# Performance work log

Measured on AMD Instinct MI355X. Metric: run time of the kernel, lower is better.

The kernel has to match this reference:

```python
import jax, jax.numpy as jnp
import numpy as np

B, T, V, D = 2048, 32, 1024, 256


def setup_inputs() -> dict:
    key = jax.random.key(0)
    k1, k2 = jax.random.split(key)
    input = jax.random.normal(k1, (B, T, D), dtype=jnp.float32)
    codebook = jax.random.normal(k2, (T, V, D), dtype=jnp.float32)
    return {"input": input, "codebook": codebook}


def reference(input, codebook):
    # input: [B, T, D]; codebook: [T, V, D]
    x = jnp.moveaxis(input, 1, 0)  # [T, B, D]
    # Squared euclidean distances; argmin is invariant to the sqrt in cdist.
    x2 = jnp.sum(x * x, axis=-1)[..., None]            # [T, B, 1]
    c2 = jnp.sum(codebook * codebook, axis=-1)[:, None, :]  # [T, 1, V]
    xc = jnp.einsum('tbd,tvd->tbv', x, codebook)       # [T, B, V]
    d2 = x2 - 2.0 * xc + c2                            # [T, B, V]
    idxes_ = jnp.argmin(d2, axis=-1)                   # [T, B]
    idxes = idxes_.T                                   # [B, T]
    # Direct per-token gather: embed[b, t] = codebook[t, idxes[b, t]]
    embed_ = codebook[jnp.arange(T)[:, None], idxes_]  # [T, B, D]
    embed = jnp.moveaxis(embed_, 0, 1)                 # [B, T, D]
    return embed, idxes
```

## Files before the change

kernel.cpp:

```cpp
#include <hip/hip_runtime.h>
#include <hip/hip_bf16.h>


#define B_ 2048
#define T_ 32
#define V_ 1024
#define D_ 256
#define BT 128
#define VT 128
#define NVT 8
#define CAND_MAX 1280
#define MARGIN 8.0f

typedef __attribute__((ext_vector_type(8))) short short8;
typedef __attribute__((ext_vector_type(4))) float f32x4;

__device__ __forceinline__ unsigned short f2bf(float f) {
    unsigned u = __builtin_bit_cast(unsigned, f);
    unsigned r = u + 0x7FFFu + ((u >> 16) & 1u);
    return (unsigned short)(r >> 16);
}

__device__ __forceinline__ short8 pack8(float4 a, float4 b) {
    short8 r;
    r[0] = (short)f2bf(a.x); r[1] = (short)f2bf(a.y);
    r[2] = (short)f2bf(a.z); r[3] = (short)f2bf(a.w);
    r[4] = (short)f2bf(b.x); r[5] = (short)f2bf(b.y);
    r[6] = (short)f2bf(b.z); r[7] = (short)f2bf(b.w);
    return r;
}

__global__ void prep_kernel(const float* __restrict__ cb, float* __restrict__ c2,
                            unsigned short* __restrict__ cbb) {
    const int wave = threadIdx.x >> 6, lane = threadIdx.x & 63;
    const int row = blockIdx.x * 4 + wave;
    const float4 v4 = *(const float4*)(cb + (size_t)row * D_ + lane * 4);
    float s = v4.x * v4.x + v4.y * v4.y + v4.z * v4.z + v4.w * v4.w;
    #pragma unroll
    for (int off = 32; off; off >>= 1) s += __shfl_down(s, off, 64);
    if (lane == 0) c2[row] = s;

    ushort4 b4;
    b4.x = f2bf(v4.x); b4.y = f2bf(v4.y); b4.z = f2bf(v4.z); b4.w = f2bf(v4.w);
    *(ushort4*)(cbb + (size_t)row * D_ + lane * 4) = b4;
}

__global__ void c2_kernel(const float* __restrict__ cb, float* __restrict__ c2) {
    const int row = blockIdx.x * 4 + (threadIdx.x >> 6);
    const int lane = threadIdx.x & 63;
    const float4 v = ((const float4*)(cb + (size_t)row * D_))[lane];
    float s = v.x * v.x + v.y * v.y + v.z * v.z + v.w * v.w;
    #pragma unroll
    for (int off = 32; off; off >>= 1) s += __shfl_down(s, off, 64);
    if (lane == 0) c2[row] = s;
}

__global__ __launch_bounds__(256, 2)
void vq_kernel(const float* __restrict__ x, const float* __restrict__ cb,
               const float* __restrict__ c2, const unsigned short* __restrict__ cbb,
               float* __restrict__ out, int use_bf) {
    const int t  = blockIdx.x;
    const int b0 = blockIdx.y * BT;

    __shared__ short8 A_lds[4096];
    __shared__ float  minPart[BT * 2];
    __shared__ unsigned long long result[BT];
    __shared__ unsigned s_cand[CAND_MAX];
    __shared__ unsigned s_cnt;

    const int tid = threadIdx.x;
    const int wave = tid >> 6, lane = tid & 63;
    const int wm = wave & 1, wn = wave >> 1;
    const int q = lane >> 4, ln = lane & 15;

    if (tid < BT) result[tid] = ~0ULL;
    minPart[tid] = 3.4e38f;
    if (tid == 0) s_cnt = 0;

    #pragma unroll
    for (int i = 0; i < 16; ++i) {
        int gid = i * 256 + tid, r = gid >> 5, g = gid & 31;
        const float4* src = (const float4*)(x + (((size_t)(b0 + r)) * T_ + t) * D_ + g * 8);
        A_lds[r * 32 + (g ^ (r & 15))] = pack8(src[0], src[1]);
    }

    const unsigned short* bb = cbb + ((size_t)t * V_ + wn * 64 + ln) * D_ + q * 8;
    const float*          fb = cb  + ((size_t)t * V_ + wn * 64 + ln) * D_ + q * 8;

    auto loadB = [&](int vt, int kc, short8 (&dst)[4]) {
        #pragma unroll
        for (int nt = 0; nt < 4; ++nt) {
            const int off = (vt * VT + nt * 16) * D_ + kc * 32;
            if (use_bf) {
                dst[nt] = *(const short8*)(bb + off);
            } else {
                const float4* s = (const float4*)(fb + off);
                dst[nt] = pack8(s[0], s[1]);
            }
        }
    };

    short8 bA[4], bB[4];
    loadB(0, 0, bA);
    __syncthreads();

    const int abase = (wm * 64 + ln) * 32;

    for (int vt = 0; vt < NVT; ++vt) {
        f32x4 acc[4][4];
        #pragma unroll
        for (int mt = 0; mt < 4; ++mt)
            #pragma unroll
            for (int nt = 0; nt < 4; ++nt) acc[mt][nt] = (f32x4){0.f, 0.f, 0.f, 0.f};

        #pragma unroll
        for (int kh = 0; kh < 4; ++kh) {
            const int kc0 = kh * 2, kc1 = kh * 2 + 1;

            loadB(vt, kc1, bB);
            {
                short8 af[4];
                #pragma unroll
                for (int mt = 0; mt < 4; ++mt)
                    af[mt] = A_lds[abase + mt * 512 + ((kc0 * 4 + q) ^ ln)];
                #pragma unroll
                for (int mt = 0; mt < 4; ++mt)
                    #pragma unroll
                    for (int nt = 0; nt < 4; ++nt)
                        acc[mt][nt] = __builtin_amdgcn_mfma_f32_16x16x32_bf16(af[mt], bA[nt], acc[mt][nt], 0, 0, 0);
            }
            if (!(vt == NVT - 1 && kh == 3)) {
                int nv = vt, nk = kc0 + 2;
                if (kh == 3) { nv = vt + 1; nk = 0; }
                loadB(nv, nk, bA);
            }
            {
                short8 af[4];
                #pragma unroll
                for (int mt = 0; mt < 4; ++mt)
                    af[mt] = A_lds[abase + mt * 512 + ((kc1 * 4 + q) ^ ln)];
                #pragma unroll
                for (int mt = 0; mt < 4; ++mt)
                    #pragma unroll
                    for (int nt = 0; nt < 4; ++nt)
                        acc[mt][nt] = __builtin_amdgcn_mfma_f32_16x16x32_bf16(af[mt], bB[nt], acc[mt][nt], 0, 0, 0);
            }
        }

        const float* c2p = c2 + t * V_ + vt * VT + wn * 64 + ln;
        float cc[4];
        #pragma unroll
        for (int nt = 0; nt < 4; ++nt) cc[nt] = c2p[nt * 16];

        #pragma unroll
        for (int mt = 0; mt < 4; ++mt)
            #pragma unroll
            for (int i = 0; i < 4; ++i) {
                float mn = 3.4e38f;
                #pragma unroll
                for (int nt = 0; nt < 4; ++nt)
                    mn = fminf(mn, fmaf(-2.0f, acc[mt][nt][i], cc[nt]));
                mn = fminf(mn, __shfl_xor(mn, 1, 64));
                mn = fminf(mn, __shfl_xor(mn, 2, 64));
                mn = fminf(mn, __shfl_xor(mn, 4, 64));
                mn = fminf(mn, __shfl_xor(mn, 8, 64));
                if (ln == 0) {
                    int r = wm * 64 + mt * 16 + q * 4 + i;
                    minPart[r * 2 + wn] = fminf(minPart[r * 2 + wn], mn);
                }
            }
        __syncthreads();

        #pragma unroll
        for (int mt = 0; mt < 4; ++mt)
            #pragma unroll
            for (int i = 0; i < 4; ++i) {
                int r = wm * 64 + mt * 16 + q * 4 + i;
                float2 mp = *(const float2*)&minPart[r * 2];
                float thr = fminf(mp.x, mp.y) + MARGIN;
                #pragma unroll
                for (int nt = 0; nt < 4; ++nt) {
                    float s = fmaf(-2.0f, acc[mt][nt][i], cc[nt]);
                    if (s < thr) {
                        int v = vt * VT + wn * 64 + nt * 16 + ln;
                        unsigned pos = atomicAdd(&s_cnt, 1u);
                        if (pos < CAND_MAX) s_cand[pos] = (unsigned)((r << 10) | v);
                    }
                }
            }
    }

    __syncthreads();
    const unsigned ncand = min(s_cnt, (unsigned)CAND_MAX);
    const int grp = tid >> 4, l16 = tid & 15;
    for (unsigned ci = grp; ci < ncand; ci += 16) {
        const unsigned e = s_cand[ci];
        const int row = e >> 10, v = e & 1023;
        const float* xr = x + (((size_t)(b0 + row)) * T_ + t) * D_ + l16 * 16;
        const float* cr = cb + ((size_t)t * V_ + v) * D_ + l16 * 16;
        float dot = 0.f;
        #pragma unroll
        for (int j = 0; j < 4; ++j) {
            float4 a = *(const float4*)(xr + j * 4);
            float4 b = *(const float4*)(cr + j * 4);
            dot = fmaf(a.x, b.x, dot); dot = fmaf(a.y, b.y, dot);
            dot = fmaf(a.z, b.z, dot); dot = fmaf(a.w, b.w, dot);
        }
        dot += __shfl_xor(dot, 1, 64);
        dot += __shfl_xor(dot, 2, 64);
        dot += __shfl_xor(dot, 4, 64);
        dot += __shfl_xor(dot, 8, 64);
        if (l16 == 0) {
            float sc = fmaf(-2.0f, dot, c2[t * V_ + v]);
            unsigned u = __builtin_bit_cast(unsigned, sc);
            u = (u & 0x80000000u) ? ~u : (u | 0x80000000u);
            atomicMin(&result[row], ((unsigned long long)u << 32) | (unsigned)v);
        }
    }
    __syncthreads();

    if (tid < BT)
        out[(size_t)B_ * T_ * D_ + (size_t)(b0 + tid) * T_ + t] =
            (float)(int)(result[tid] & 1023u);

    const int w = tid >> 6, gl = tid & 63;
    #pragma unroll
    for (int i = 0; i < 32; ++i) {
        const int row = w * 32 + i;
        const int idx = (int)(result[row] & 1023u);
        const float4 src = *(const float4*)(cb + ((size_t)t * V_ + idx) * D_ + gl * 4);
        *(float4*)(out + (((size_t)(b0 + row)) * T_ + t) * D_ + gl * 4) = src;
    }
}

extern "C" void kernel_launch(void* const* d_in, const int* in_sizes, int n_in,
                              void* d_out, int out_size, void* d_ws, size_t ws_size,
                              hipStream_t stream) {
    const float* x  = (const float*)d_in[0];
    const float* cb = (const float*)d_in[1];
    float* out = (float*)d_out;
    float* c2  = (float*)d_ws;
    unsigned short* cbb = (unsigned short*)((char*)d_ws + 131072);
    const size_t NEED = 131072 + (size_t)T_ * V_ * D_ * 2;
    const int use_bf = (ws_size >= NEED) ? 1 : 0;

    if (use_bf) prep_kernel<<<dim3(T_ * V_ / 4), 256, 0, stream>>>(cb, c2, cbb);
    else        c2_kernel<<<dim3(T_ * V_ / 4), 256, 0, stream>>>(cb, c2);
    vq_kernel<<<dim3(T_, B_ / BT), 256, 0, stream>>>(x, cb, c2, cbb, out, use_bf);
}
```

Baseline: 295.4 us.

## Halve batch tile, raise occupancy, aggregate candidate atomics per wave

Cuts the per-block batch tile from 128 to 64 rows, halving the accumulator registers and LDS per block, and raises launch bounds to 4 blocks per CU to get more latency hiding. The codebook B-fragment loads switch to a simple per-k double buffer over a fully unrolled loop. Candidate collection now uses a wave ballot with a single atomicAdd per wave in place of one atomic per lane. The trade-off is that each codebook tile is re-read by twice as many blocks, which raises global/L2 traffic, and the smaller candidate buffer may overflow more easily.

```diff
diff --git a/kernel.cpp b/kernel.cpp
--- a/kernel.cpp
+++ b/kernel.cpp
@@ -6,10 +6,10 @@
 #define T_ 32
 #define V_ 1024
 #define D_ 256
-#define BT 128
+#define BT 64
 #define VT 128
 #define NVT 8
-#define CAND_MAX 1280
+#define CAND_MAX 1024
 #define MARGIN 8.0f
 
 typedef __attribute__((ext_vector_type(8))) short short8;
@@ -55,14 +55,14 @@
     if (lane == 0) c2[row] = s;
 }
 
-__global__ __launch_bounds__(256, 2)
+__global__ __launch_bounds__(256, 4)
 void vq_kernel(const float* __restrict__ x, const float* __restrict__ cb,
                const float* __restrict__ c2, const unsigned short* __restrict__ cbb,
                float* __restrict__ out, int use_bf) {
     const int t  = blockIdx.x;
     const int b0 = blockIdx.y * BT;
 
-    __shared__ short8 A_lds[4096];
+    __shared__ short8 A_lds[BT * 32];
     __shared__ float  minPart[BT * 2];
     __shared__ unsigned long long result[BT];
     __shared__ unsigned s_cand[CAND_MAX];
@@ -74,11 +74,11 @@
     const int q = lane >> 4, ln = lane & 15;
 
     if (tid < BT) result[tid] = ~0ULL;
-    minPart[tid] = 3.4e38f;
+    if (tid < BT * 2) minPart[tid] = 3.4e38f;
     if (tid == 0) s_cnt = 0;
 
     #pragma unroll
-    for (int i = 0; i < 16; ++i) {
+    for (int i = 0; i < 8; ++i) {
         int gid = i * 256 + tid, r = gid >> 5, g = gid & 31;
         const float4* src = (const float4*)(x + (((size_t)(b0 + r)) * T_ + t) * D_ + g * 8);
         A_lds[r * 32 + (g ^ (r & 15))] = pack8(src[0], src[1]);
@@ -100,51 +100,35 @@
         }
     };
 
-    short8 bA[4], bB[4];
-    loadB(0, 0, bA);
+    short8 bufs[2][4];
+    loadB(0, 0, bufs[0]);
     __syncthreads();
 
-    const int abase = (wm * 64 + ln) * 32;
-
+    const int abase = (wm * 32 + ln) * 32;
+
+    #pragma unroll
     for (int vt = 0; vt < NVT; ++vt) {
-        f32x4 acc[4][4];
-        #pragma unroll
-        for (int mt = 0; mt < 4; ++mt)
+        f32x4 acc[2][4];
+        #pragma unroll
+        for (int mt = 0; mt < 2; ++mt)
             #pragma unroll
             for (int nt = 0; nt < 4; ++nt) acc[mt][nt] = (f32x4){0.f, 0.f, 0.f, 0.f};
 
         #pragma unroll
-        for (int kh = 0; kh < 4; ++kh) {
-            const int kc0 = kh * 2, kc1 = kh * 2 + 1;
-
-            loadB(vt, kc1, bB);
-            {
-                short8 af[4];
+        for (int kc = 0; kc < 8; ++kc) {
+            if (!(vt == NVT - 1 && kc == 7)) {
+                const int s1 = vt * 8 + kc + 1;
+                loadB(s1 >> 3, s1 & 7, bufs[(kc + 1) & 1]);
+            }
+            short8 af[2];
+            af[0] = A_lds[abase + ((kc * 4 + q) ^ ln)];
+            af[1] = A_lds[abase + 512 + ((kc * 4 + q) ^ ln)];
+            #pragma unroll
+            for (int mt = 0; mt < 2; ++mt)
                 #pragma unroll
-                for (int mt = 0; mt < 4; ++mt)
-                    af[mt] = A_lds[abase + mt * 512 + ((kc0 * 4 + q) ^ ln)];
-                #pragma unroll
-                for (int mt = 0; mt < 4; ++mt)
-                    #pragma unroll
-                    for (int nt = 0; nt < 4; ++nt)
-                        acc[mt][nt] = __builtin_amdgcn_mfma_f32_16x16x32_bf16(af[mt], bA[nt], acc[mt][nt], 0, 0, 0);
-            }
-            if (!(vt == NVT - 1 && kh == 3)) {
-                int nv = vt, nk = kc0 + 2;
-                if (kh == 3) { nv = vt + 1; nk = 0; }
-                loadB(nv, nk, bA);
-            }
-            {
-                short8 af[4];
-                #pragma unroll
-                for (int mt = 0; mt < 4; ++mt)
-                    af[mt] = A_lds[abase + mt * 512 + ((kc1 * 4 + q) ^ ln)];
-                #pragma unroll
-                for (int mt = 0; mt < 4; ++mt)
-                    #pragma unroll
-                    for (int nt = 0; nt < 4; ++nt)
-                        acc[mt][nt] = __builtin_amdgcn_mfma_f32_16x16x32_bf16(af[mt], bB[nt], acc[mt][nt], 0, 0, 0);
-            }
+                for (int nt = 0; nt < 4; ++nt)
+                    acc[mt][nt] = __builtin_amdgcn_mfma_f32_16x16x32_bf16(
+                        af[mt], bufs[kc & 1][nt], acc[mt][nt], 0, 0, 0);
         }
 
         const float* c2p = c2 + t * V_ + vt * VT + wn * 64 + ln;
@@ -153,7 +137,7 @@
         for (int nt = 0; nt < 4; ++nt) cc[nt] = c2p[nt * 16];
 
         #pragma unroll
-        for (int mt = 0; mt < 4; ++mt)
+        for (int mt = 0; mt < 2; ++mt)
             #pragma unroll
             for (int i = 0; i < 4; ++i) {
                 float mn = 3.4e38f;
@@ -165,26 +149,36 @@
                 mn = fminf(mn, __shfl_xor(mn, 4, 64));
                 mn = fminf(mn, __shfl_xor(mn, 8, 64));
                 if (ln == 0) {
-                    int r = wm * 64 + mt * 16 + q * 4 + i;
+                    int r = wm * 32 + mt * 16 + q * 4 + i;
                     minPart[r * 2 + wn] = fminf(minPart[r * 2 + wn], mn);
                 }
             }
         __syncthreads();
 
         #pragma unroll
-        for (int mt = 0; mt < 4; ++mt)
+        for (int mt = 0; mt < 2; ++mt)
             #pragma unroll
             for (int i = 0; i < 4; ++i) {
-                int r = wm * 64 + mt * 16 + q * 4 + i;
+                const int r = wm * 32 + mt * 16 + q * 4 + i;
                 float2 mp = *(const float2*)&minPart[r * 2];
                 float thr = fminf(mp.x, mp.y) + MARGIN;
                 #pragma unroll
                 for (int nt = 0; nt < 4; ++nt) {
                     float s = fmaf(-2.0f, acc[mt][nt][i], cc[nt]);
-                    if (s < thr) {
-                        int v = vt * VT + wn * 64 + nt * 16 + ln;
-                        unsigned pos = atomicAdd(&s_cnt, 1u);
-                        if (pos < CAND_MAX) s_cand[pos] = (unsigned)((r << 10) | v);
+                    const bool pred = (s < thr);
+                    unsigned long long m = __ballot(pred);
+                    if (m) {
+                        const int first = __ffsll((unsigned long long)m) - 1;
+                        unsigned base = 0;
+                        if (lane == first) base = atomicAdd(&s_cnt, (unsigned)__popcll(m));
+                        base = __shfl(base, first, 64);
+                        if (pred) {
+                            unsigned pos = base + (unsigned)__popcll(m & ((1ull << lane) - 1ull));
+                            if (pos < CAND_MAX) {
+                                int v = vt * VT + wn * 64 + nt * 16 + ln;
+                                s_cand[pos] = (unsigned)((r << 10) | v);
+                            }
+                        }
                     }
                 }
             }
@@ -223,13 +217,12 @@
         out[(size_t)B_ * T_ * D_ + (size_t)(b0 + tid) * T_ + t] =
             (float)(int)(result[tid] & 1023u);
 
-    const int w = tid >> 6, gl = tid & 63;
-    #pragma unroll
-    for (int i = 0; i < 32; ++i) {
-        const int row = w * 32 + i;
+    #pragma unroll
+    for (int i = 0; i < 16; ++i) {
+        const int row = wave * 16 + i;
         const int idx = (int)(result[row] & 1023u);
-        const float4 src = *(const float4*)(cb + ((size_t)t * V_ + idx) * D_ + gl * 4);
-        *(float4*)(out + (((size_t)(b0 + row)) * T_ + t) * D_ + gl * 4) = src;
+        const float4 src = *(const float4*)(cb + ((size_t)t * V_ + idx) * D_ + lane * 4);
+        *(float4*)(out + (((size_t)(b0 + row)) * T_ + t) * D_ + lane * 4) = src;
     }
 }
 
```

Measured after the change: 307.2 us. 1.04x slower.
